# Performance work log

Hardware: AMD Instinct MI355X
Metric: run time of the kernel (lower is better)

## Reference

```python
import jax, jax.numpy as jnp
import numpy as np

DIMS = 1024
STATE = 2 * DIMS
EPS = 1e-8


def _rmsnorm(v, scale):
    # norm = ||v||_2 * d^{-1/2}
    d = v.shape[-1]
    n = jnp.sqrt(jnp.sum(v * v, axis=-1, keepdims=True)) * (d ** -0.5)
    return scale * v / (n + EPS)


def setup_inputs() -> dict:
    key = jax.random.key(0)
    ks = jax.random.split(key, 5)
    x = jax.random.normal(ks[0], (4, 2048, DIMS), dtype=jnp.float32)
    ls_scale = jnp.ones((DIMS // 2,), dtype=jnp.float32)
    rs_scale = jnp.ones((DIMS // 2,), dtype=jnp.float32)
    split_scale = jnp.full((DIMS,), 0.1, dtype=jnp.float32)
    sk = (1.0 / DIMS) ** 0.5
    Wk = jax.random.uniform(ks[1], (DIMS, STATE), jnp.float32, -sk, sk)
    Wugg = jax.random.uniform(ks[2], (DIMS, 3 * STATE), jnp.float32, -sk, sk)
    so = (1.0 / STATE) ** 0.5
    Wout = jax.random.uniform(ks[3], (STATE, DIMS), jnp.float32, -so, so)
    return {"x": x, "ls_scale": ls_scale, "rs_scale": rs_scale,
            "split_scale": split_scale, "Wk": Wk, "Wugg": Wugg, "Wout": Wout}


def reference(x, ls_scale, rs_scale, split_scale, Wk, Wugg, Wout):
    residual = x
    # RMS_split norm (output_dim=None)
    xl, xr = jnp.split(x, 2, axis=-1)
    xn = jnp.concatenate([_rmsnorm(xl, ls_scale), _rmsnorm(xr, rs_scale)], axis=-1)
    xn = xn * split_scale

    K = jax.nn.sigmoid(xn @ Wk)                      # [B,S,STATE]
    u, g_in, g_out = jnp.split(xn @ Wugg, 3, axis=-1)
    u = u * jax.nn.sigmoid(g_in) * (1.0 - K)

    # linear recurrence: h_0 = u_0; h_t = K_{t-1} * h_{t-1} + u_t
    a = jnp.concatenate([jnp.ones_like(K[..., :1, :]), K[..., :-1, :]], axis=-2)

    def combine(lhs, rhs):
        aL, bL = lhs
        aR, bR = rhs
        return (aL * aR, bL * aR + bR)

    _, h = jax.lax.associative_scan(combine, (a, u), axis=1)
    outputs = h * jax.nn.sigmoid(g_out)
    y = outputs @ Wout
    return y + residual
```

## Files before the change

### kernel.cpp

```cpp
#include <hip/hip_runtime.h>
#include <hip/hip_bf16.h>
#include <hip/hip_fp8.h>
#include <stdint.h>

#define DIMS 1024
#define STATE 2048
#define BATCH 4
#define SEQ 2048
#define TOKENS 8192
#define N1 8192
#define NCHUNK 16
#define CHUNKL (SEQ / NCHUNK)

typedef __hip_bfloat16 bf16;
typedef unsigned char u8;
typedef __attribute__((ext_vector_type(8))) short bf16x8;
typedef __attribute__((ext_vector_type(4))) float f32x4;
typedef __attribute__((ext_vector_type(16))) float f32x16;
typedef __attribute__((ext_vector_type(2))) long v2i64;

#define XN_SCALE 32.0f
#define W1_SCALE 256.0f
#define INV_SCALE (1.0f / 8192.0f)

__device__ __forceinline__ float sigmoidf_(float x) {
  return 1.0f / (1.0f + __expf(-x));
}

__device__ __forceinline__ u8 to_fp8(float f) {
  __hip_fp8_e4m3 h(f);
  return h.__x;
}

__device__ __forceinline__ int kperm(int k) {
  return (k & ~24) | ((k & 8) << 1) | ((k & 16) >> 1);
}

__device__ __forceinline__ void async_copy16(const void* g, void* l) {
  __builtin_amdgcn_global_load_lds(
      (const __attribute__((address_space(1))) void*)(uintptr_t)g,
      (__attribute__((address_space(3))) void*)(uint32_t)(uintptr_t)l,
      16, 0, 0);
}

__device__ __forceinline__ int swz32(int row, int kc) {
  int line = row >> 1;
  int sub = ((row & 1) << 2) | kc;
  return (line << 3) | (sub ^ (line & 7));
}
__device__ __forceinline__ void swz32_dec(int c, int& row, int& kc) {
  int line = c >> 3;
  int sub = (c & 7) ^ (line & 7);
  row = (line << 1) | (sub >> 2);
  kc = sub & 3;
}
__device__ __forceinline__ int swz64(int row, int kc) {
  return (row << 3) | (kc ^ (row & 7));
}
__device__ __forceinline__ void swz64_dec(int c, int& row, int& kc) {
  row = c >> 3;
  kc = (c & 7) ^ (row & 7);
}

__global__ __launch_bounds__(256) void transpose_bf16_kernel(
    const float* __restrict__ W, bf16* __restrict__ Wt, int K, int N) {
  __shared__ float tile[32][33];
  int tx = threadIdx.x & 31;
  int ty = threadIdx.x >> 5;
  long col = (long)blockIdx.x * 32 + tx;
  long rowb = (long)blockIdx.y * 32;
#pragma unroll
  for (int i = 0; i < 32; i += 8)
    tile[ty + i][tx] = W[(rowb + ty + i) * N + col];
  __syncthreads();
  long ocol = rowb + tx;
  long orow = (long)blockIdx.x * 32 + ty;
#pragma unroll
  for (int i = 0; i < 32; i += 8)
    Wt[(orow + i) * K + ocol] = __float2bfloat16(tile[tx][ty + i]);
}

__global__ __launch_bounds__(256) void transpose_fp8_kernel(
    const float* __restrict__ W, u8* __restrict__ Wt, int K, int N) {
  __shared__ float tile[32][33];
  int tx = threadIdx.x & 31;
  int ty = threadIdx.x >> 5;
  long col = (long)blockIdx.x * 32 + tx;
  long rowb = (long)blockIdx.y * 32;
#pragma unroll
  for (int i = 0; i < 32; i += 8)
    tile[ty + i][tx] = W[(rowb + ty + i) * N + col];
  __syncthreads();
  long ocol = rowb + kperm(tx);
  long orow = (long)blockIdx.x * 32 + ty;
#pragma unroll
  for (int i = 0; i < 32; i += 8)
    Wt[(orow + i) * K + ocol] = to_fp8(tile[tx][ty + i] * W1_SCALE);
}

__global__ __launch_bounds__(256) void rmsnorm_kernel(
    const float* __restrict__ x, const float* __restrict__ ls,
    const float* __restrict__ rs, const float* __restrict__ ss,
    u8* __restrict__ xn8) {
  int token = blockIdx.x;
  int tid = threadIdx.x;
  const float4* xt = (const float4*)(x + (long)token * DIMS);
  float4 v = xt[tid];
  float s = v.x * v.x + v.y * v.y + v.z * v.z + v.w * v.w;
#pragma unroll
  for (int d = 32; d > 0; d >>= 1) s += __shfl_down(s, d);
  __shared__ float parts[4];
  if ((tid & 63) == 0) parts[tid >> 6] = s;
  __syncthreads();
  int j = tid * 4;
  bool left = j < 512;
  float sum = left ? (parts[0] + parts[1]) : (parts[2] + parts[3]);
  float n = sqrtf(sum * (1.0f / 512.0f));
  float inv = 1.0f / (n + 1e-8f);
  const float4* sc = (const float4*)(left ? ls : rs);
  float4 g = sc[left ? tid : tid - 128];
  float4 p = ((const float4*)ss)[tid];
  u8 q[4];
  q[0] = to_fp8(v.x * g.x * inv * p.x * XN_SCALE);
  q[1] = to_fp8(v.y * g.y * inv * p.y * XN_SCALE);
  q[2] = to_fp8(v.z * g.z * inv * p.z * XN_SCALE);
  q[3] = to_fp8(v.w * g.w * inv * p.w * XN_SCALE);
  *(uint32_t*)(xn8 + (long)token * DIMS + kperm(j)) = *(uint32_t*)q;
}

__device__ __forceinline__ void g1f8_stage(const u8* __restrict__ A,
                                           const u8* __restrict__ Bt,
                                           long arow0, long brow0, int k0,
                                           int wave, int lane, u8* As, u8* Bs) {
  const int K = DIMS;
#pragma unroll
  for (int i = 0; i < 4; i++) {
    int c = (wave * 4 + i) * 64 + lane;
    int row, kc; swz32_dec(c, row, kc);
    async_copy16(A + (arow0 + row) * K + k0 + kc * 16, (char*)As + (wave * 4 + i) * 1024);
  }
#pragma unroll
  for (int i = 0; i < 2; i++) {
    int c = (wave * 2 + i) * 64 + lane;
    int row, kc; swz32_dec(c, row, kc);
    async_copy16(Bt + (brow0 + row) * K + k0 + kc * 16, (char*)Bs + (wave * 2 + i) * 1024);
  }
}

__global__ __launch_bounds__(256, 2) void gemm1_fp8(
    const u8* __restrict__ A, const u8* __restrict__ Bt, bf16* __restrict__ C) {
  __shared__ __align__(16) u8 As0[256 * 64], As1[256 * 64];
  __shared__ __align__(16) u8 Bs0[128 * 64], Bs1[128 * 64];
  int tid = threadIdx.x;
  int lane = tid & 63, wave = tid >> 6;
  int wm = wave & 1, wn = wave >> 1;
  long arow0 = (long)blockIdx.y * 256;
  long brow0 = (long)blockIdx.x * 128;
  int m_lane = lane & 31, q4 = lane >> 5;
  f32x16 acc[4][2] = {};

  g1f8_stage(A, Bt, arow0, brow0, 0, wave, lane, As0, Bs0);
  __syncthreads();

  for (int it = 0; it < 16; it += 2) {
    {
      v2i64 af[2][4], bfr[2][2];
#pragma unroll
      for (int p = 0; p < 2; p++) {
#pragma unroll
        for (int mt = 0; mt < 4; mt++)
          af[p][mt] = *(const v2i64*)(As0 + swz32(wm * 128 + mt * 32 + m_lane, p * 2 + q4) * 16);
#pragma unroll
        for (int nt = 0; nt < 2; nt++)
          bfr[p][nt] = *(const v2i64*)(Bs0 + swz32(wn * 64 + nt * 32 + m_lane, p * 2 + q4) * 16);
      }
      g1f8_stage(A, Bt, arow0, brow0, (it + 1) * 64, wave, lane, As1, Bs1);
#pragma unroll
      for (int p = 0; p < 2; p++)
#pragma unroll
        for (int mt = 0; mt < 4; mt++)
#pragma unroll
          for (int nt = 0; nt < 2; nt++) {
            acc[mt][nt] = __builtin_amdgcn_mfma_f32_32x32x16_fp8_fp8(bfr[p][nt][0], af[p][mt][0], acc[mt][nt], 0, 0, 0);
            acc[mt][nt] = __builtin_amdgcn_mfma_f32_32x32x16_fp8_fp8(bfr[p][nt][1], af[p][mt][1], acc[mt][nt], 0, 0, 0);
          }
      __syncthreads();
    }
    {
      v2i64 af[2][4], bfr[2][2];
#pragma unroll
      for (int p = 0; p < 2; p++) {
#pragma unroll
        for (int mt = 0; mt < 4; mt++)
          af[p][mt] = *(const v2i64*)(As1 + swz32(wm * 128 + mt * 32 + m_lane, p * 2 + q4) * 16);
#pragma unroll
        for (int nt = 0; nt < 2; nt++)
          bfr[p][nt] = *(const v2i64*)(Bs1 + swz32(wn * 64 + nt * 32 + m_lane, p * 2 + q4) * 16);
      }
      if (it + 2 < 16)
        g1f8_stage(A, Bt, arow0, brow0, (it + 2) * 64, wave, lane, As0, Bs0);
#pragma unroll
      for (int p = 0; p < 2; p++)
#pragma unroll
        for (int mt = 0; mt < 4; mt++)
#pragma unroll
          for (int nt = 0; nt < 2; nt++) {
            acc[mt][nt] = __builtin_amdgcn_mfma_f32_32x32x16_fp8_fp8(bfr[p][nt][0], af[p][mt][0], acc[mt][nt], 0, 0, 0);
            acc[mt][nt] = __builtin_amdgcn_mfma_f32_32x32x16_fp8_fp8(bfr[p][nt][1], af[p][mt][1], acc[mt][nt], 0, 0, 0);
          }
      __syncthreads();
    }
  }
#pragma unroll
  for (int mt = 0; mt < 4; mt++) {
    long row = arow0 + wm * 128 + mt * 32 + m_lane;
#pragma unroll
    for (int nt = 0; nt < 2; nt++) {
#pragma unroll
      for (int g = 0; g < 4; g++) {
        long col = brow0 + wn * 64 + nt * 32 + g * 8 + q4 * 4;
        bf16 tmp[4];
#pragma unroll
        for (int j = 0; j < 4; j++)
          tmp[j] = __float2bfloat16(acc[mt][nt][g * 4 + j] * INV_SCALE);
        *(uint2*)(C + row * N1 + col) = *(uint2*)tmp;
      }
    }
  }
}

__device__ __forceinline__ void g2_stage(const bf16* __restrict__ A,
                                         const bf16* __restrict__ Bt,
                                         long arow0, long brow0, int k0, int K,
                                         int wave, int lane, bf16* As, bf16* Bs) {
#pragma unroll
  for (int i = 0; i < 4; i++) {
    int c = (wave * 4 + i) * 64 + lane;
    int row, kc; swz64_dec(c, row, kc);
    async_copy16(A + (arow0 + row) * K + k0 + kc * 8, (char*)As + (wave * 4 + i) * 1024);
    async_copy16(Bt + (brow0 + row) * K + k0 + kc * 8, (char*)Bs + (wave * 4 + i) * 1024);
  }
}

__global__ __launch_bounds__(256) void gemm2_resid(
    const bf16* __restrict__ A, const bf16* __restrict__ Bt,
    float* __restrict__ C, const float* __restrict__ resid) {
  __shared__ __align__(16) bf16 As0[128 * 64], As1[128 * 64];
  __shared__ __align__(16) bf16 Bs0[128 * 64], Bs1[128 * 64];
  const int K = STATE, N = DIMS;
  int tid = threadIdx.x;
  int lane = tid & 63, wave = tid >> 6;
  int wm = wave & 1, wn = wave >> 1;
  long arow0 = (long)blockIdx.y * 128;
  long brow0 = (long)blockIdx.x * 128;
  int r = lane & 15, q = lane >> 4;
  f32x4 acc[4][4] = {};

  g2_stage(A, Bt, arow0, brow0, 0, K, wave, lane, As0, Bs0);
  __syncthreads();

  for (int it = 0; it < 32; it += 2) {
    {
      const bf16x8* AsV = (const bf16x8*)As0;
      const bf16x8* BsV = (const bf16x8*)Bs0;
      bf16x8 af[2][4], bfr[2][4];
#pragma unroll
      for (int ks = 0; ks < 2; ks++) {
#pragma unroll
        for (int mt = 0; mt < 4; mt++) af[ks][mt] = AsV[swz64(wm * 64 + mt * 16 + r, ks * 4 + q)];
#pragma unroll
        for (int nt = 0; nt < 4; nt++) bfr[ks][nt] = BsV[swz64(wn * 64 + nt * 16 + r, ks * 4 + q)];
      }
      g2_stage(A, Bt, arow0, brow0, (it + 1) * 64, K, wave, lane, As1, Bs1);
#pragma unroll
      for (int ks = 0; ks < 2; ks++)
#pragma unroll
        for (int mt = 0; mt < 4; mt++)
#pragma unroll
          for (int nt = 0; nt < 4; nt++)
            acc[mt][nt] = __builtin_amdgcn_mfma_f32_16x16x32_bf16(bfr[ks][nt], af[ks][mt], acc[mt][nt], 0, 0, 0);
      __syncthreads();
    }
    {
      const bf16x8* AsV = (const bf16x8*)As1;
      const bf16x8* BsV = (const bf16x8*)Bs1;
      bf16x8 af[2][4], bfr[2][4];
#pragma unroll
      for (int ks = 0; ks < 2; ks++) {
#pragma unroll
        for (int mt = 0; mt < 4; mt++) af[ks][mt] = AsV[swz64(wm * 64 + mt * 16 + r, ks * 4 + q)];
#pragma unroll
        for (int nt = 0; nt < 4; nt++) bfr[ks][nt] = BsV[swz64(wn * 64 + nt * 16 + r, ks * 4 + q)];
      }
      if (it + 2 < 32)
        g2_stage(A, Bt, arow0, brow0, (it + 2) * 64, K, wave, lane, As0, Bs0);
#pragma unroll
      for (int ks = 0; ks < 2; ks++)
#pragma unroll
        for (int mt = 0; mt < 4; mt++)
#pragma unroll
          for (int nt = 0; nt < 4; nt++)
            acc[mt][nt] = __builtin_amdgcn_mfma_f32_16x16x32_bf16(bfr[ks][nt], af[ks][mt], acc[mt][nt], 0, 0, 0);
      __syncthreads();
    }
  }

#pragma unroll
  for (int mt = 0; mt < 4; mt++) {
    long row = arow0 + wm * 64 + mt * 16 + r;
#pragma unroll
    for (int nt = 0; nt < 4; nt++) {
      long col = brow0 + wn * 64 + nt * 16 + q * 4;
      float4 rv = *(const float4*)(resid + row * N + col);
      float4 ov;
      ov.x = acc[mt][nt][0] + rv.x;
      ov.y = acc[mt][nt][1] + rv.y;
      ov.z = acc[mt][nt][2] + rv.z;
      ov.w = acc[mt][nt][3] + rv.w;
      *(float4*)(C + row * N + col) = ov;
    }
  }
}


__global__ __launch_bounds__(256) void chunk_summary_kernel(
    const bf16* __restrict__ C1, float* __restrict__ carryA,
    float* __restrict__ carryU) {
  int b = blockIdx.x;
  int ch = blockIdx.y * 256 + threadIdx.x;
  int chunk = blockIdx.z;
  int t0 = chunk * CHUNKL;
  long base = ((long)b * SEQ) * N1 + ch;
  float kp = 0.0f;
  if (chunk != 0) kp = __bfloat162float(C1[base + (long)(t0 - 1) * N1]);
  float a_first = (chunk == 0) ? 1.0f : sigmoidf_(kp);
  float A = 1.0f, U = 0.0f;
#pragma unroll 8
  for (int t = t0; t < t0 + CHUNKL; t++) {
    long off = base + (long)t * N1;
    float kraw = __bfloat162float(C1[off]);
    float uraw = __bfloat162float(C1[off + 2048]);
    float gin  = __bfloat162float(C1[off + 4096]);
    float a = (t == t0) ? a_first : sigmoidf_(kp);
    float sK = sigmoidf_(kraw);
    float u = uraw * sigmoidf_(gin) * (1.0f - sK);
    A *= a;
    U = a * U + u;
    kp = kraw;
  }
  int cidx = (b * NCHUNK + chunk) * STATE + ch;
  carryA[cidx] = A;
  carryU[cidx] = U;
}

__global__ __launch_bounds__(256) void carry_scan_kernel(
    const float* __restrict__ carryA, const float* __restrict__ carryU,
    float* __restrict__ carryIn) {
  int idx = blockIdx.x * 256 + threadIdx.x;
  int b = idx >> 11;
  int ch = idx & 2047;
  float h = 0.0f;
#pragma unroll
  for (int c = 0; c < NCHUNK; c++) {
    int cidx = (b * NCHUNK + c) * STATE + ch;
    carryIn[cidx] = h;
    h = carryA[cidx] * h + carryU[cidx];
  }
}

__global__ __launch_bounds__(256) void scan_chunk_kernel(
    const bf16* __restrict__ C1, const float* __restrict__ carryIn,
    bf16* __restrict__ out) {
  int b = blockIdx.x;
  int c0 = blockIdx.y * 32;
  int chunk = blockIdx.z;
  int tstart = chunk * CHUNKL;
  __shared__ float a_s[32][65], u_s[32][65], h_s[32][65];
  int tid = threadIdx.x;
  int lane = tid & 63, wave = tid >> 6;
  int cc = tid & 31;
  int tq = tid >> 5;

  float carryH[8], carryK[8];
#pragma unroll
  for (int i = 0; i < 8; i++) {
    int ch = c0 + wave * 8 + i;
    carryH[i] = carryIn[(b * NCHUNK + chunk) * STATE + ch];
    carryK[i] = (chunk == 0)
                    ? 1.0f
                    : sigmoidf_(__bfloat162float(
                          C1[((long)(b * SEQ + tstart - 1)) * N1 + ch]));
  }

  float g_r[8];
  for (int t0 = tstart; t0 < tstart + CHUNKL; t0 += 64) {
#pragma unroll
    for (int i = 0; i < 8; i++) {
      int t = tq * 8 + i;
      long rowoff = ((long)(b * SEQ + t0 + t)) * N1 + c0 + cc;
      float kraw = __bfloat162float(C1[rowoff]);
      float uraw = __bfloat162float(C1[rowoff + 2048]);
      float gin  = __bfloat162float(C1[rowoff + 4096]);
      float gout = __bfloat162float(C1[rowoff + 6144]);
      float aK = sigmoidf_(kraw);
      a_s[cc][t] = aK;
      u_s[cc][t] = uraw * sigmoidf_(gin) * (1.0f - aK);
      g_r[i] = sigmoidf_(gout);
    }
    __syncthreads();
#pragma unroll
    for (int i = 0; i < 8; i++) {
      int ch = wave * 8 + i;
      float aK = a_s[ch][lane];
      float u = u_s[ch][lane];
      float a = __shfl_up(aK, 1);
      if (lane == 0) a = carryK[i];
      float A = a, U = u;
#pragma unroll
      for (int d = 1; d < 64; d <<= 1) {
        float Au = __shfl_up(A, d);
        float Uu = __shfl_up(U, d);
        if (lane >= d) { U += A * Uu; A *= Au; }
      }
      float h = U + A * carryH[i];
      carryH[i] = __shfl(h, 63);
      carryK[i] = __shfl(aK, 63);
      h_s[ch][lane] = h;
    }
    __syncthreads();
#pragma unroll
    for (int i = 0; i < 8; i++) {
      int t = tq * 8 + i;
      out[((long)(b * SEQ + t0 + t)) * STATE + c0 + cc] =
          __float2bfloat16(h_s[cc][t] * g_r[i]);
    }
    __syncthreads();
  }
}

extern "C" void kernel_launch(void* const* d_in, const int* in_sizes, int n_in,
                              void* d_out, int out_size, void* d_ws, size_t ws_size,
                              hipStream_t stream) {
  const float* x    = (const float*)d_in[0];
  const float* ls   = (const float*)d_in[1];
  const float* rs   = (const float*)d_in[2];
  const float* ss   = (const float*)d_in[3];
  const float* Wk   = (const float*)d_in[4];
  const float* Wugg = (const float*)d_in[5];
  const float* Wout = (const float*)d_in[6];
  float* out = (float*)d_out;

  char* ws = (char*)d_ws;
  u8*   W1f8 = (u8*)ws;
  bf16* W2t  = (bf16*)(ws + 8388608);
  u8*   xn8  = (u8*)(ws + 8388608 + 4194304);
  bf16* C1   = (bf16*)(ws + 8388608 + 4194304 + 8388608);
  bf16* sco  = (bf16*)(ws + 8388608 + 4194304 + 8388608 + 134217728);
  float* carryA  = (float*)xn8;
  float* carryU  = carryA + BATCH * NCHUNK * STATE;
  float* carryIn = carryU + BATCH * NCHUNK * STATE;

  transpose_fp8_kernel<<<dim3(STATE / 32, DIMS / 32), 256, 0, stream>>>(Wk, W1f8, DIMS, STATE);
  transpose_fp8_kernel<<<dim3(3 * STATE / 32, DIMS / 32), 256, 0, stream>>>(
      Wugg, W1f8 + (long)STATE * DIMS, DIMS, 3 * STATE);
  transpose_bf16_kernel<<<dim3(DIMS / 32, STATE / 32), 256, 0, stream>>>(Wout, W2t, STATE, DIMS);

  rmsnorm_kernel<<<TOKENS, 256, 0, stream>>>(x, ls, rs, ss, xn8);

  gemm1_fp8<<<dim3(N1 / 128, TOKENS / 256), 256, 0, stream>>>(xn8, W1f8, C1);

  chunk_summary_kernel<<<dim3(BATCH, STATE / 256, NCHUNK), 256, 0, stream>>>(
      C1, carryA, carryU);
  carry_scan_kernel<<<dim3(BATCH * STATE / 256), 256, 0, stream>>>(
      carryA, carryU, carryIn);
  scan_chunk_kernel<<<dim3(BATCH, STATE / 32, NCHUNK), 256, 0, stream>>>(
      C1, carryIn, sco);

  gemm2_resid<<<dim3(DIMS / 128, TOKENS / 128), 256, 0, stream>>>(
      sco, W2t, out, x);
}
```

Baseline: 404.8 us.

## Interleave K/u/gin/gout columns of GEMM1 output for vectorized scan loads

Reorders the fused weight rows so that GEMM1 writes the four streams (K, u, g_in, g_out) for each channel as four adjacent bf16 values. The chunk summary and scan kernels then fetch all four with a single 8-byte load instead of four strided 2-byte loads. The GEMM itself is unchanged apart from the column permutation applied during the weight transpose. The cost is stride-4 coalescing per thread across channels, which makes each wave's access wider but reduces the number of load instructions and separate cache lines touched.

```diff
diff --git a/kernel.cpp b/kernel.cpp
--- a/kernel.cpp
+++ b/kernel.cpp
@@ -14,6 +14,7 @@
 
 typedef __hip_bfloat16 bf16;
 typedef unsigned char u8;
+typedef unsigned short u16;
 typedef __attribute__((ext_vector_type(8))) short bf16x8;
 typedef __attribute__((ext_vector_type(4))) float f32x4;
 typedef __attribute__((ext_vector_type(16))) float f32x16;
@@ -30,6 +31,12 @@
 __device__ __forceinline__ u8 to_fp8(float f) {
   __hip_fp8_e4m3 h(f);
   return h.__x;
+}
+
+__device__ __forceinline__ float b2f(u16 v) {
+  union { uint32_t u; float f; } w;
+  w.u = ((uint32_t)v) << 16;
+  return w.f;
 }
 
 __device__ __forceinline__ int kperm(int k) {
@@ -81,7 +88,7 @@
 }
 
 __global__ __launch_bounds__(256) void transpose_fp8_kernel(
-    const float* __restrict__ W, u8* __restrict__ Wt, int K, int N) {
+    const float* __restrict__ W, u8* __restrict__ Wt, int K, int N, int stream_base) {
   __shared__ float tile[32][33];
   int tx = threadIdx.x & 31;
   int ty = threadIdx.x >> 5;
@@ -94,8 +101,11 @@
   long ocol = rowb + kperm(tx);
   long orow = (long)blockIdx.x * 32 + ty;
 #pragma unroll
-  for (int i = 0; i < 32; i += 8)
-    Wt[(orow + i) * K + ocol] = to_fp8(tile[tx][ty + i] * W1_SCALE);
+  for (int i = 0; i < 32; i += 8) {
+    long n = orow + i;
+    long dstrow = ((n & 2047) << 2) | (stream_base + (n >> 11));
+    Wt[dstrow * K + ocol] = to_fp8(tile[tx][ty + i] * W1_SCALE);
+  }
 }
 
 __global__ __launch_bounds__(256) void rmsnorm_kernel(
@@ -330,17 +340,18 @@
   int ch = blockIdx.y * 256 + threadIdx.x;
   int chunk = blockIdx.z;
   int t0 = chunk * CHUNKL;
-  long base = ((long)b * SEQ) * N1 + ch;
+  const bf16* base = C1 + ((long)b * SEQ) * N1 + ch * 4;
   float kp = 0.0f;
-  if (chunk != 0) kp = __bfloat162float(C1[base + (long)(t0 - 1) * N1]);
+  if (chunk != 0) kp = __bfloat162float(base[(long)(t0 - 1) * N1]);
   float a_first = (chunk == 0) ? 1.0f : sigmoidf_(kp);
   float A = 1.0f, U = 0.0f;
 #pragma unroll 8
   for (int t = t0; t < t0 + CHUNKL; t++) {
-    long off = base + (long)t * N1;
-    float kraw = __bfloat162float(C1[off]);
-    float uraw = __bfloat162float(C1[off + 2048]);
-    float gin  = __bfloat162float(C1[off + 4096]);
+    union { uint2 u2; u16 h[4]; } w;
+    w.u2 = *(const uint2*)(base + (long)t * N1);
+    float kraw = b2f(w.h[0]);
+    float uraw = b2f(w.h[1]);
+    float gin  = b2f(w.h[2]);
     float a = (t == t0) ? a_first : sigmoidf_(kp);
     float sK = sigmoidf_(kraw);
     float u = uraw * sigmoidf_(gin) * (1.0f - sK);
@@ -389,7 +400,7 @@
     carryK[i] = (chunk == 0)
                     ? 1.0f
                     : sigmoidf_(__bfloat162float(
-                          C1[((long)(b * SEQ + tstart - 1)) * N1 + ch]));
+                          C1[((long)(b * SEQ + tstart - 1)) * N1 + ch * 4]));
   }
 
   float g_r[8];
@@ -397,11 +408,12 @@
 #pragma unroll
     for (int i = 0; i < 8; i++) {
       int t = tq * 8 + i;
-      long rowoff = ((long)(b * SEQ + t0 + t)) * N1 + c0 + cc;
-      float kraw = __bfloat162float(C1[rowoff]);
-      float uraw = __bfloat162float(C1[rowoff + 2048]);
-      float gin  = __bfloat162float(C1[rowoff + 4096]);
-      float gout = __bfloat162float(C1[rowoff + 6144]);
+      union { uint2 u2; u16 h[4]; } w;
+      w.u2 = *(const uint2*)(C1 + ((long)(b * SEQ + t0 + t)) * N1 + (c0 + cc) * 4);
+      float kraw = b2f(w.h[0]);
+      float uraw = b2f(w.h[1]);
+      float gin  = b2f(w.h[2]);
+      float gout = b2f(w.h[3]);
       float aK = sigmoidf_(kraw);
       a_s[cc][t] = aK;
       u_s[cc][t] = uraw * sigmoidf_(gin) * (1.0f - aK);
@@ -460,9 +472,10 @@
   float* carryU  = carryA + BATCH * NCHUNK * STATE;
   float* carryIn = carryU + BATCH * NCHUNK * STATE;
 
-  transpose_fp8_kernel<<<dim3(STATE / 32, DIMS / 32), 256, 0, stream>>>(Wk, W1f8, DIMS, STATE);
+  transpose_fp8_kernel<<<dim3(STATE / 32, DIMS / 32), 256, 0, stream>>>(
+      Wk, W1f8, DIMS, STATE, 0);
   transpose_fp8_kernel<<<dim3(3 * STATE / 32, DIMS / 32), 256, 0, stream>>>(
-      Wugg, W1f8 + (long)STATE * DIMS, DIMS, 3 * STATE);
+      Wugg, W1f8, DIMS, 3 * STATE, 1);
   transpose_bf16_kernel<<<dim3(DIMS / 32, STATE / 32), 256, 0, stream>>>(Wout, W2t, STATE, DIMS);
 
   rmsnorm_kernel<<<TOKENS, 256, 0, stream>>>(x, ls, rs, ss, xn8);
```

Result: faster. 387.3 us (-4.3%).
